# Optimization experiments

Hardware: AMD Instinct MI355X
Metric: run time of the kernel (lower is better)

The kernel has to match this reference:

```python
import jax, jax.numpy as jnp
import numpy as np

B, DEC, F = 64, 12, 32        # batch, decoder steps, decoder feature size
L, H = 2, 512                 # gru layers, hidden size
E, T = 96, 4                  # encoder seq len, target size


def gru_cell(x, h, Wi, Wh, bi, bh):
    # PyTorch GRUCell math
    gi = x @ Wi.T + bi
    gh = h @ Wh.T + bh
    i_r, i_z, i_n = jnp.split(gi, 3, axis=-1)
    h_r, h_z, h_n = jnp.split(gh, 3, axis=-1)
    r = jax.nn.sigmoid(i_r + h_r)
    z = jax.nn.sigmoid(i_z + h_z)
    n = jnp.tanh(i_n + r * h_n)
    return (1.0 - z) * n + z * h


def setup_inputs() -> dict:
    key = jax.random.key(0)
    ks = jax.random.split(key, 12)
    s = lambda k, shape: jax.random.normal(k, shape, jnp.float32) * 0.02
    return {
        "inputs": jax.random.normal(ks[0], (B, DEC, F), jnp.float32),
        "hidden": jax.random.normal(ks[1], (L, B, H), jnp.float32) * 0.1,
        "enc_outputs": jax.random.normal(ks[2], (B, E, H), jnp.float32),
        "target_indices": jnp.arange(T, dtype=jnp.int32),
        "W_attn": s(ks[3], (H, 2 * H)),
        "b_attn": jnp.zeros((H,), jnp.float32),
        "v_attn": s(ks[4], (H,)),
        "gru_Wi0": s(ks[5], (3 * H, F + H)),
        "gru_Wh0": s(ks[6], (3 * H, H)),
        "gru_bi0": jnp.zeros((3 * H,), jnp.float32),
        "gru_bh0": jnp.zeros((3 * H,), jnp.float32),
        "gru_Wi1": s(ks[7], (3 * H, H)),
        "gru_Wh1": s(ks[8], (3 * H, H)),
        "gru_bi1": jnp.zeros((3 * H,), jnp.float32),
        "gru_bh1": jnp.zeros((3 * H,), jnp.float32),
        "W_out": s(ks[9], (T, 2 * H + F)),
        "b_out": jnp.zeros((T,), jnp.float32),
    }


def reference(inputs, hidden, enc_outputs, target_indices,
              W_attn, b_attn, v_attn,
              gru_Wi0, gru_Wh0, gru_bi0, gru_bh0,
              gru_Wi1, gru_Wh1, gru_bi1, gru_bh1,
              W_out, b_out):
    Hs = hidden.shape[-1]
    Wa_h, Wa_e = W_attn[:, :Hs], W_attn[:, Hs:]
    # encoder projection of the attn linear is constant over timesteps
    enc_proj = jnp.einsum('beh,gh->beg', enc_outputs, Wa_e)  # [B,E,H]
    layers = ((gru_Wi0, gru_Wh0, gru_bi0, gru_bh0),
              (gru_Wi1, gru_Wh1, gru_bi1, gru_bh1))

    def step(carry, x_t):
        h, cur = carry                     # h: [L,B,H], cur: [B,F]
        hl = h[-1]                         # final-layer hidden [B,H]
        energy = jnp.tanh(enc_proj + (hl @ Wa_h.T + b_attn)[:, None, :])
        w = jax.nn.softmax(energy @ v_attn, axis=1)          # [B,E]
        ws = jnp.einsum('be,beh->bh', w, enc_outputs)        # [B,H]
        x = jnp.concatenate([cur, ws], axis=-1)              # [B,F+H]
        new_h = []
        for l, (Wi, Wh, bi, bh) in enumerate(layers):
            hn = gru_cell(x, h[l], Wi, Wh, bi, bh)
            new_h.append(hn)
            x = hn
        out = jnp.concatenate([x, ws, cur], axis=-1) @ W_out.T + b_out  # [B,T]
        nxt = x_t.at[:, target_indices].set(out)  # feed prediction back
        return (jnp.stack(new_h), nxt), out

    xs = jnp.swapaxes(inputs, 0, 1)  # [DEC,B,F]
    (_, _), outs = jax.lax.scan(step, (hidden, inputs[:, 0, :]), xs)
    return jnp.swapaxes(outs, 0, 1)  # [B,DEC,T]
```

## Files before the change

### kernel.cpp

```cpp
#include <hip/hip_runtime.h>
#include <hip/hip_fp16.h>

#define NB   64
#define NDEC 12
#define NF   32
#define NH   512
#define NE   96
#define NT   4
#define KI0  (NF + NH)
#define KOUT (2*NH + NF)

typedef _Float16 half8_t __attribute__((ext_vector_type(8)));
typedef float   float4_t __attribute__((ext_vector_type(4)));

__device__ __forceinline__ float fast_tanh(float x) {
    x = fminf(fmaxf(x, -15.f), 15.f);
    float e = __expf(2.f * x);
    return (e - 1.f) / (e + 1.f);
}
__device__ __forceinline__ float fast_sig(float x) {
    return 1.f / (1.f + __expf(-x));
}

__global__ __launch_bounds__(256) void k_prep(
    const float* __restrict__ Wi0, const float* __restrict__ Wh0,
    const float* __restrict__ Wi1, const float* __restrict__ Wh1,
    const float* __restrict__ Wout, const float* __restrict__ Wattn,
    const float* __restrict__ hidden, const float* __restrict__ inputs,
    __half* __restrict__ Wi0h, __half* __restrict__ Wh0h,
    __half* __restrict__ Wi1h, __half* __restrict__ Wh1h,
    __half* __restrict__ Wouth, __half* __restrict__ WahH,
    __half* __restrict__ WaeH,
    float* __restrict__ h0row, float* __restrict__ h1row,
    __half* __restrict__ h0h, __half* __restrict__ h1h,
    __half* __restrict__ xcat0)
{
    int i = blockIdx.x*256 + threadIdx.x;
    const int n0 = 1536*KI0, n1 = 1536*512, n4 = 4*KOUT, n5 = 512*512;
    if (i < n0) { Wi0h[i] = __float2half_rn(Wi0[i]); return; }  i -= n0;
    if (i < n1) { Wh0h[i] = __float2half_rn(Wh0[i]); return; }  i -= n1;
    if (i < n1) { Wi1h[i] = __float2half_rn(Wi1[i]); return; }  i -= n1;
    if (i < n1) { Wh1h[i] = __float2half_rn(Wh1[i]); return; }  i -= n1;
    if (i < n4) { Wouth[i] = __float2half_rn(Wout[i]); return; } i -= n4;
    if (i < n5) {
        int g = i >> 9, k = i & 511;
        WahH[i] = __float2half_rn(Wattn[(size_t)g*1024 + k]);
        return;
    }
    i -= n5;
    if (i < n5) {
        int g = i >> 9, k = i & 511;
        WaeH[i] = __float2half_rn(Wattn[(size_t)g*1024 + 512 + k]);
        return;
    }
    i -= n5;
    if (i < NB*NH) {
        int b = i >> 9, k = i & 511;
        float v0 = hidden[b*NH + k];
        float v1 = hidden[NB*NH + b*NH + k];
        h0row[b*NH + k] = v0;  h0h[b*NH + k] = __float2half_rn(v0);
        h1row[b*NH + k] = v1;  h1h[b*NH + k] = __float2half_rn(v1);
        return;
    }
    i -= NB*NH;
    if (i < NB*NF) {
        int b = i >> 5, k = i & 31;
        xcat0[(size_t)b*KI0 + k] = __float2half_rn(inputs[b*NDEC*NF + k]);
    }
}

__global__ __launch_bounds__(256) void k_encproj(const float* __restrict__ enc,
                                                 const __half* __restrict__ WaeH,
                                                 __half* __restrict__ encph) {
    int x = blockIdx.x;
    int by = x >> 3, bx = x & 7;
    int t = threadIdx.x, w = t >> 6, lane = t & 63;
    int mr = lane & 15, kq = lane >> 4;
    int m = by*64 + w*16 + mr;
    const float* arow = enc + (size_t)m*NH;
    float4_t acc[4] = {{0.f,0.f,0.f,0.f},{0.f,0.f,0.f,0.f},
                       {0.f,0.f,0.f,0.f},{0.f,0.f,0.f,0.f}};
    for (int kb = 0; kb < NH; kb += 32) {
        int k = kb + kq*8;
        float4 a0 = *(const float4*)(arow + k);
        float4 a1 = *(const float4*)(arow + k + 4);
        half8_t a;
        a[0] = (_Float16)a0.x; a[1] = (_Float16)a0.y;
        a[2] = (_Float16)a0.z; a[3] = (_Float16)a0.w;
        a[4] = (_Float16)a1.x; a[5] = (_Float16)a1.y;
        a[6] = (_Float16)a1.z; a[7] = (_Float16)a1.w;
        #pragma unroll
        for (int j = 0; j < 4; ++j) {
            int n = bx*64 + j*16 + mr;
            half8_t b = *(const half8_t*)(WaeH + (size_t)n*NH + k);
            acc[j] = __builtin_amdgcn_mfma_f32_16x16x32_f16(a, b, acc[j], 0, 0, 0);
        }
    }
    #pragma unroll
    for (int j = 0; j < 4; ++j) {
        int col = bx*64 + j*16 + mr;
        #pragma unroll
        for (int r = 0; r < 4; ++r) {
            int row = by*64 + w*16 + kq*4 + r;
            encph[(size_t)row*NH + col] = __float2half_rn(acc[j][r]);
        }
    }
}

__global__ __launch_bounds__(1024) void k_att(
    const __half* __restrict__ WahH, const float* __restrict__ battn,
    const __half* __restrict__ h1h,
    float* __restrict__ attcT)
{
    int blk = blockIdx.x, t = threadIdx.x;
    int w = t >> 6, lane = t & 63;
    int mr = lane & 15, kq = lane >> 4;
    int rt = (blk & 7)*4 + (blk >> 3);
    int rt16 = rt*16;
    int bq = w >> 2, wq = w & 3;
    __shared__ float parts[4][4][16][17];

    float bat = battn[rt16 + (t & 15)];
    const __half* arow = WahH + (size_t)(rt16 + mr)*NH;
    const __half* brow = h1h + (size_t)(bq*16 + mr)*NH;
    int kb0 = wq*128 + kq*8;
    half8_t a0 = *(const half8_t*)(arow + kb0);
    half8_t b0 = *(const half8_t*)(brow + kb0);
    half8_t a1 = *(const half8_t*)(arow + kb0 + 32);
    half8_t b1 = *(const half8_t*)(brow + kb0 + 32);
    half8_t a2 = *(const half8_t*)(arow + kb0 + 64);
    half8_t b2 = *(const half8_t*)(brow + kb0 + 64);
    half8_t a3 = *(const half8_t*)(arow + kb0 + 96);
    half8_t b3 = *(const half8_t*)(brow + kb0 + 96);
    float4_t acc = {0.f,0.f,0.f,0.f};
    acc = __builtin_amdgcn_mfma_f32_16x16x32_f16(a0, b0, acc, 0, 0, 0);
    acc = __builtin_amdgcn_mfma_f32_16x16x32_f16(a1, b1, acc, 0, 0, 0);
    acc = __builtin_amdgcn_mfma_f32_16x16x32_f16(a2, b2, acc, 0, 0, 0);
    acc = __builtin_amdgcn_mfma_f32_16x16x32_f16(a3, b3, acc, 0, 0, 0);
    #pragma unroll
    for (int r = 0; r < 4; ++r) parts[bq][wq][kq*4 + r][mr] = acc[r];
    __syncthreads();

    int sub = t >> 8, tt = t & 255;
    int jl = tt & 15, bl = tt >> 4;
    float v = parts[sub][0][jl][bl] + parts[sub][1][jl][bl]
            + parts[sub][2][jl][bl] + parts[sub][3][jl][bl];
    attcT[(size_t)(sub*16 + bl)*NH + rt16 + jl] = v + bat;
}

__global__ __launch_bounds__(1024) void k_soft(
    const float* __restrict__ inputs, const int* __restrict__ tgt,
    const float* __restrict__ vattn,
    const float* __restrict__ attcT,
    const __half* __restrict__ encph, const float* __restrict__ enc,
    const __half* __restrict__ Wouth, const float* __restrict__ bout,
    const __half* __restrict__ Wh0h, const __half* __restrict__ Wh1h,
    const __half* __restrict__ h0h, const __half* __restrict__ h1h,
    float* __restrict__ ghb,
    const __half* __restrict__ xcatP,
    __half* __restrict__ xcatC,
    float* __restrict__ out, int s)
{
    int blk = blockIdx.x, t = threadIdx.x;
    int lane = t & 63, widx = t >> 6;
    __shared__ float vs[NH], atts[NH];
    __shared__ float pes[NE], combA[NH], combB[NH];
    __shared__ float invD_sh;
    __shared__ float parts[4][4][16][17];

    if (blk >= 64 && blk < 256) {
        int gblk = blk - 64;
        int rt = (gblk & 7)*24 + (gblk >> 3);
        int layer = (rt >= 96) ? 1 : 0;
        int rloc = (rt - layer*96) * 16;
        int bq = widx >> 2, wq = widx & 3;
        int mr = lane & 15, kq = lane >> 4;
        const __half* Wh = layer ? Wh1h : Wh0h;
        const __half* Xh = layer ? h1h : h0h;
        const __half* arow = Wh + (size_t)(rloc + mr)*NH;
        const __half* brow = Xh + (size_t)(bq*16 + mr)*NH;
        int kb0 = wq*128 + kq*8;
        half8_t a0 = *(const half8_t*)(arow + kb0);
        half8_t b0 = *(const half8_t*)(brow + kb0);
        half8_t a1 = *(const half8_t*)(arow + kb0 + 32);
        half8_t b1 = *(const half8_t*)(brow + kb0 + 32);
        half8_t a2 = *(const half8_t*)(arow + kb0 + 64);
        half8_t b2 = *(const half8_t*)(brow + kb0 + 64);
        half8_t a3 = *(const half8_t*)(arow + kb0 + 96);
        half8_t b3 = *(const half8_t*)(brow + kb0 + 96);
        float4_t acc = {0.f,0.f,0.f,0.f};
        acc = __builtin_amdgcn_mfma_f32_16x16x32_f16(a0, b0, acc, 0, 0, 0);
        acc = __builtin_amdgcn_mfma_f32_16x16x32_f16(a1, b1, acc, 0, 0, 0);
        acc = __builtin_amdgcn_mfma_f32_16x16x32_f16(a2, b2, acc, 0, 0, 0);
        acc = __builtin_amdgcn_mfma_f32_16x16x32_f16(a3, b3, acc, 0, 0, 0);
        #pragma unroll
        for (int r = 0; r < 4; ++r) parts[bq][wq][kq*4 + r][mr] = acc[r];
        __syncthreads();
        int sub = t >> 8, tt = t & 255;
        int jl = tt >> 4, bl = tt & 15;
        float v = parts[sub][0][jl][bl] + parts[sub][1][jl][bl]
                + parts[sub][2][jl][bl] + parts[sub][3][jl][bl];
        ghb[((size_t)layer*3*NH + rloc + jl)*NB + sub*16 + bl] = v;
        return;
    }

    if (blk == 256) {
        if (s == 0 || widx >= 4) return;
        int mr = lane & 15, kq = lane >> 4;
        int b = widx*16 + mr;
        const __half* h1b = h1h + (size_t)b*NH;
        const __half* xcb = xcatP + (size_t)b*KI0;
        int ar = (mr < 4) ? mr : 3;
        const __half* arow = Wouth + (size_t)ar*KOUT;
        float4_t acc = {0.f,0.f,0.f,0.f};
        for (int kb = 0; kb < KOUT; kb += 32) {
            int k = kb + kq*8;
            half8_t a = *(const half8_t*)(arow + k);
            const __half* bp = (k < NH)   ? (h1b + k)
                             : (k < 2*NH) ? (xcb + NF + (k - NH))
                                          : (xcb + (k - 2*NH));
            half8_t bb = *(const half8_t*)bp;
            acc = __builtin_amdgcn_mfma_f32_16x16x32_f16(a, bb, acc, 0, 0, 0);
        }
        float o0 = __shfl(acc[0], mr) + bout[0];
        float o1 = __shfl(acc[1], mr) + bout[1];
        float o2 = __shfl(acc[2], mr) + bout[2];
        float o3 = __shfl(acc[3], mr) + bout[3];
        if (kq == 0) {
            *(float4*)(out + (size_t)b*(NDEC*NT) + (s-1)*NT) = make_float4(o0,o1,o2,o3);
        }
        int t0 = tgt[0], t1 = tgt[1], t2 = tgt[2], t3 = tgt[3];
        const float* ip = inputs + (size_t)b*(NDEC*NF) + (s-1)*NF;
        half8_t hv;
        #pragma unroll
        for (int i = 0; i < 8; ++i) {
            int f = kq*8 + i;
            float v = ip[f];
            v = (f == t0) ? o0 : (f == t1) ? o1 : (f == t2) ? o2 : (f == t3) ? o3 : v;
            hv[i] = (_Float16)__float2half_rn(v);
        }
        *(half8_t*)(xcatC + (size_t)b*KI0 + kq*8) = hv;
        return;
    }

    int b = blk;
    if (t < NH) { vs[t] = vattn[t]; atts[t] = attcT[(size_t)b*NH + t]; }

    float er[48];
    {
        int k = t & 511, half = t >> 9;
        const float* eb = enc + ((size_t)b*NE + half*48)*NH + k;
        #pragma unroll
        for (int e = 0; e < 48; ++e) er[e] = eb[(size_t)e*NH];
    }
    __syncthreads();

    {
        float ar[8], vr[8];
        #pragma unroll
        for (int i = 0; i < 8; ++i) { ar[i] = atts[lane*8 + i]; vr[i] = vs[lane*8 + i]; }
        for (int it = 0; it < 6; ++it) {
            int e = widx + it*16;
            const __half* ep = encph + ((size_t)(b*NE + e))*NH + lane*8;
            uint4 u = *(const uint4*)ep;
            __half2 p0 = *(__half2*)&u.x, p1 = *(__half2*)&u.y;
            __half2 p2 = *(__half2*)&u.z, p3 = *(__half2*)&u.w;
            float2 f0 = __half22float2(p0), f1 = __half22float2(p1);
            float2 f2 = __half22float2(p2), f3 = __half22float2(p3);
            float sacc;
            sacc  = fast_tanh(f0.x + ar[0]) * vr[0];
            sacc += fast_tanh(f0.y + ar[1]) * vr[1];
            sacc += fast_tanh(f1.x + ar[2]) * vr[2];
            sacc += fast_tanh(f1.y + ar[3]) * vr[3];
            sacc += fast_tanh(f2.x + ar[4]) * vr[4];
            sacc += fast_tanh(f2.y + ar[5]) * vr[5];
            sacc += fast_tanh(f3.x + ar[6]) * vr[6];
            sacc += fast_tanh(f3.y + ar[7]) * vr[7];
            #pragma unroll
            for (int off = 32; off; off >>= 1) sacc += __shfl_down(sacc, off);
            if (lane == 0) pes[e] = __expf(sacc);
        }
    }
    __syncthreads();

    if (t < 64) {
        float v = pes[t] + ((t < 32) ? pes[64 + t] : 0.f);
        #pragma unroll
        for (int off = 32; off; off >>= 1) v += __shfl_down(v, off);
        if (t == 0) invD_sh = 1.f / v;
    }
    __syncthreads();

    {
        int k = t & 511, half = t >> 9;
        float acc = 0.f;
        #pragma unroll
        for (int e = 0; e < 48; ++e) acc += pes[half*48 + e] * er[e];
        if (half == 0) combA[k] = acc; else combB[k] = acc;
    }
    __syncthreads();
    if (t < NH) {
        float v = (combA[t] + combB[t]) * invD_sh;
        xcatC[(size_t)b*KI0 + NF + t] = __float2half_rn(v);
    }
}

__global__ __launch_bounds__(768) void k_gru(
    const __half* __restrict__ Wi,
    const float* __restrict__ bi, const float* __restrict__ bh,
    const __half* __restrict__ xh, int K,
    const float* __restrict__ ghbL,
    const float* __restrict__ hold,
    float* __restrict__ hnew,
    __half* __restrict__ hnewh)
{
    int blk = blockIdx.x, t = threadIdx.x;
    int w = t >> 6, lane = t & 63;
    int mr = lane & 15, kq = lane >> 4;
    int sblk = (blk & 7)*16 + (blk >> 3);
    int jg = sblk >> 2, bq = sblk & 3;
    int j0 = jg*16, b0 = bq*16;
    __shared__ float parts[3][4][16][17];

    float ghr = 0.f, ghz = 0.f, ghn = 0.f, hp = 0.f;
    float biR = 0.f, bhR = 0.f, biZ = 0.f, bhZ = 0.f, biN = 0.f, bhN = 0.f;
    if (t < 256) {
        int jl = t >> 4, bl = t & 15;
        int j = j0 + jl, b = b0 + bl;
        ghr = ghbL[(size_t)(0*NH + j)*NB + b];
        ghz = ghbL[(size_t)(1*NH + j)*NB + b];
        ghn = ghbL[(size_t)(2*NH + j)*NB + b];
        hp  = hold[(size_t)b*NH + j];
        biR = bi[j];        bhR = bh[j];
        biZ = bi[NH + j];   bhZ = bh[NH + j];
        biN = bi[2*NH + j]; bhN = bh[2*NH + j];
    }

    int gate = w >> 2, c = w & 3;
    int nsteps = K >> 5;
    int rem = nsteps & 3;
    int base = c*(nsteps >> 2) + ((c < rem) ? c : rem);
    int cnt  = (nsteps >> 2) + ((c < rem) ? 1 : 0);
    const __half* arow = Wi + (size_t)(gate*NH + j0 + mr)*K;
    const __half* brow = xh + (size_t)(b0 + mr)*K;
    float4_t acc = {0.f,0.f,0.f,0.f};
    for (int i2 = 0; i2 < cnt; ++i2) {
        int kb = (base + i2)*32;
        half8_t a = *(const half8_t*)(arow + kb + kq*8);
        half8_t b = *(const half8_t*)(brow + kb + kq*8);
        acc = __builtin_amdgcn_mfma_f32_16x16x32_f16(a, b, acc, 0, 0, 0);
    }
    #pragma unroll
    for (int r = 0; r < 4; ++r) parts[gate][c][kq*4 + r][mr] = acc[r];
    __syncthreads();

    if (t < 256) {
        int jl = t >> 4, bl = t & 15;
        int j = j0 + jl, b = b0 + bl;
        float S0 = parts[0][0][jl][bl] + parts[0][1][jl][bl]
                 + parts[0][2][jl][bl] + parts[0][3][jl][bl];
        float S1 = parts[1][0][jl][bl] + parts[1][1][jl][bl]
                 + parts[1][2][jl][bl] + parts[1][3][jl][bl];
        float S2 = parts[2][0][jl][bl] + parts[2][1][jl][bl]
                 + parts[2][2][jl][bl] + parts[2][3][jl][bl];
        float r = fast_sig(S0 + ghr + biR + bhR);
        float z = fast_sig(S1 + ghz + biZ + bhZ);
        float n = fast_tanh(S2 + biN + r*(ghn + bhN));
        float hv = (1.f - z)*n + z*hp;
        hnew[(size_t)b*NH + j] = hv;
        hnewh[(size_t)b*NH + j] = __float2half_rn(hv);
    }
}

__global__ __launch_bounds__(256) void k_outp(
    const __half* __restrict__ Wouth, const float* __restrict__ bout,
    const __half* __restrict__ h1h, const __half* __restrict__ xcatP,
    float* __restrict__ out)
{
    int t = threadIdx.x;
    int w = t >> 6, lane = t & 63;
    int mr = lane & 15, kq = lane >> 4;
    int b = w*16 + mr;
    const __half* h1b = h1h + (size_t)b*NH;
    const __half* xcb = xcatP + (size_t)b*KI0;
    int ar = (mr < 4) ? mr : 3;
    const __half* arow = Wouth + (size_t)ar*KOUT;
    float4_t acc = {0.f,0.f,0.f,0.f};
    for (int kb = 0; kb < KOUT; kb += 32) {
        int k = kb + kq*8;
        half8_t a = *(const half8_t*)(arow + k);
        const __half* bp = (k < NH)   ? (h1b + k)
                         : (k < 2*NH) ? (xcb + NF + (k - NH))
                                      : (xcb + (k - 2*NH));
        half8_t bb = *(const half8_t*)bp;
        acc = __builtin_amdgcn_mfma_f32_16x16x32_f16(a, bb, acc, 0, 0, 0);
    }
    float o0 = __shfl(acc[0], mr) + bout[0];
    float o1 = __shfl(acc[1], mr) + bout[1];
    float o2 = __shfl(acc[2], mr) + bout[2];
    float o3 = __shfl(acc[3], mr) + bout[3];
    if (kq == 0) {
        *(float4*)(out + (size_t)b*(NDEC*NT) + (NDEC-1)*NT) = make_float4(o0,o1,o2,o3);
    }
}

extern "C" void kernel_launch(void* const* d_in, const int* in_sizes, int n_in,
                              void* d_out, int out_size, void* d_ws, size_t ws_size,
                              hipStream_t stream) {
    const float* inputs = (const float*)d_in[0];
    const float* hidden = (const float*)d_in[1];
    const float* enc    = (const float*)d_in[2];
    const int*   tgt    = (const int*)d_in[3];
    const float* Wattn  = (const float*)d_in[4];
    const float* battn  = (const float*)d_in[5];
    const float* vattn  = (const float*)d_in[6];
    const float* Wi0    = (const float*)d_in[7];
    const float* Wh0    = (const float*)d_in[8];
    const float* bi0    = (const float*)d_in[9];
    const float* bh0    = (const float*)d_in[10];
    const float* Wi1    = (const float*)d_in[11];
    const float* Wh1    = (const float*)d_in[12];
    const float* bi1    = (const float*)d_in[13];
    const float* bh1    = (const float*)d_in[14];
    const float* Wout   = (const float*)d_in[15];
    const float* bout   = (const float*)d_in[16];
    float* out = (float*)d_out;

    float* h0row  = (float*)d_ws;
    float* h1row  = h0row + NB*NH;
    float* ghb    = h1row + NB*NH;
    float* attcT  = ghb + 2*3*NH*NB;
    __half* Wi0h  = (__half*)(attcT + NB*NH);
    __half* Wh0h  = Wi0h + 1536*KI0;
    __half* Wi1h  = Wh0h + 1536*NH;
    __half* Wh1h  = Wi1h + 1536*NH;
    __half* Wouth = Wh1h + 1536*NH;
    __half* WahH  = Wouth + 4*KOUT;
    __half* WaeH  = WahH + NH*NH;
    __half* h0h   = WaeH + NH*NH;
    __half* h1h   = h0h + NB*NH;
    __half* xcat  = h1h + NB*NH;
    __half* encph = xcat + 2*NB*KI0;

    const int prep_n = 1536*KI0 + 3*1536*NH + 4*KOUT + 2*NH*NH + NB*NH + NB*NF;
    k_prep<<<(prep_n + 255)/256, 256, 0, stream>>>(
        Wi0, Wh0, Wi1, Wh1, Wout, Wattn, hidden, inputs,
        Wi0h, Wh0h, Wi1h, Wh1h, Wouth, WahH, WaeH,
        h0row, h1row, h0h, h1h, xcat);
    k_encproj<<<768, 256, 0, stream>>>(enc, WaeH, encph);

    for (int s = 0; s < NDEC; ++s) {
        int par = s & 1;
        __half* xcatC = xcat + par*NB*KI0;
        __half* xcatP = xcat + (par^1)*NB*KI0;
        k_att<<<32, 1024, 0, stream>>>(WahH, battn, h1h, attcT);
        k_soft<<<257, 1024, 0, stream>>>(
            inputs, tgt, vattn, attcT, encph, enc, Wouth, bout,
            Wh0h, Wh1h, h0h, h1h, ghb, xcatP, xcatC, out, s);
        k_gru<<<128, 768, 0, stream>>>(Wi0h, bi0, bh0,
                                       xcatC, KI0,
                                       ghb,
                                       h0row, h0row, h0h);
        k_gru<<<128, 768, 0, stream>>>(Wi1h, bi1, bh1,
                                       h0h, NH,
                                       ghb + 3*NH*NB,
                                       h1row, h1row, h1h);
    }
    k_outp<<<1, 256, 0, stream>>>(Wouth, bout, h1h, xcat + (NB*KI0), out);
}
```

Measured before the change: 485.5 us.

## Fuse attention hidden projection into softmax kernel using transposed weights

Removes the separate k_att launch per decoder step and computes each batch row's hidden-state attention projection inside the per-batch softmax block. It uses a transposed fp16 copy of the attention weight so threads read coalesced half2 pairs, with fp32 hidden values taken from shared memory. This saves one launch and one global round trip per step. In exchange, each of the 64 batch blocks now streams the full 512x512 weight matrix on its own scalar FMA path instead of using MFMA, which adds redundant L2 traffic and latency to the critical path.

Result: slower. 541.6 us (+11.6%).

```diff
diff --git a/kernel.cpp b/kernel.cpp
--- a/kernel.cpp
+++ b/kernel.cpp
@@ -29,7 +29,7 @@
     const float* __restrict__ hidden, const float* __restrict__ inputs,
     __half* __restrict__ Wi0h, __half* __restrict__ Wh0h,
     __half* __restrict__ Wi1h, __half* __restrict__ Wh1h,
-    __half* __restrict__ Wouth, __half* __restrict__ WahH,
+    __half* __restrict__ Wouth, __half* __restrict__ WahT,
     __half* __restrict__ WaeH,
     float* __restrict__ h0row, float* __restrict__ h1row,
     __half* __restrict__ h0h, __half* __restrict__ h1h,
@@ -43,8 +43,8 @@
     if (i < n1) { Wh1h[i] = __float2half_rn(Wh1[i]); return; }  i -= n1;
     if (i < n4) { Wouth[i] = __float2half_rn(Wout[i]); return; } i -= n4;
     if (i < n5) {
-        int g = i >> 9, k = i & 511;
-        WahH[i] = __float2half_rn(Wattn[(size_t)g*1024 + k]);
+        int k = i >> 9, g = i & 511;
+        WahT[i] = __float2half_rn(Wattn[(size_t)g*1024 + k]);
         return;
     }
     i -= n5;
@@ -107,51 +107,11 @@
     }
 }
 
-__global__ __launch_bounds__(1024) void k_att(
-    const __half* __restrict__ WahH, const float* __restrict__ battn,
-    const __half* __restrict__ h1h,
-    float* __restrict__ attcT)
-{
-    int blk = blockIdx.x, t = threadIdx.x;
-    int w = t >> 6, lane = t & 63;
-    int mr = lane & 15, kq = lane >> 4;
-    int rt = (blk & 7)*4 + (blk >> 3);
-    int rt16 = rt*16;
-    int bq = w >> 2, wq = w & 3;
-    __shared__ float parts[4][4][16][17];
-
-    float bat = battn[rt16 + (t & 15)];
-    const __half* arow = WahH + (size_t)(rt16 + mr)*NH;
-    const __half* brow = h1h + (size_t)(bq*16 + mr)*NH;
-    int kb0 = wq*128 + kq*8;
-    half8_t a0 = *(const half8_t*)(arow + kb0);
-    half8_t b0 = *(const half8_t*)(brow + kb0);
-    half8_t a1 = *(const half8_t*)(arow + kb0 + 32);
-    half8_t b1 = *(const half8_t*)(brow + kb0 + 32);
-    half8_t a2 = *(const half8_t*)(arow + kb0 + 64);
-    half8_t b2 = *(const half8_t*)(brow + kb0 + 64);
-    half8_t a3 = *(const half8_t*)(arow + kb0 + 96);
-    half8_t b3 = *(const half8_t*)(brow + kb0 + 96);
-    float4_t acc = {0.f,0.f,0.f,0.f};
-    acc = __builtin_amdgcn_mfma_f32_16x16x32_f16(a0, b0, acc, 0, 0, 0);
-    acc = __builtin_amdgcn_mfma_f32_16x16x32_f16(a1, b1, acc, 0, 0, 0);
-    acc = __builtin_amdgcn_mfma_f32_16x16x32_f16(a2, b2, acc, 0, 0, 0);
-    acc = __builtin_amdgcn_mfma_f32_16x16x32_f16(a3, b3, acc, 0, 0, 0);
-    #pragma unroll
-    for (int r = 0; r < 4; ++r) parts[bq][wq][kq*4 + r][mr] = acc[r];
-    __syncthreads();
-
-    int sub = t >> 8, tt = t & 255;
-    int jl = tt & 15, bl = tt >> 4;
-    float v = parts[sub][0][jl][bl] + parts[sub][1][jl][bl]
-            + parts[sub][2][jl][bl] + parts[sub][3][jl][bl];
-    attcT[(size_t)(sub*16 + bl)*NH + rt16 + jl] = v + bat;
-}
-
 __global__ __launch_bounds__(1024) void k_soft(
     const float* __restrict__ inputs, const int* __restrict__ tgt,
-    const float* __restrict__ vattn,
-    const float* __restrict__ attcT,
+    const __half* __restrict__ WahT,
+    const float* __restrict__ battn, const float* __restrict__ vattn,
+    const float* __restrict__ h1row,
     const __half* __restrict__ encph, const float* __restrict__ enc,
     const __half* __restrict__ Wouth, const float* __restrict__ bout,
     const __half* __restrict__ Wh0h, const __half* __restrict__ Wh1h,
@@ -163,7 +123,8 @@
 {
     int blk = blockIdx.x, t = threadIdx.x;
     int lane = t & 63, widx = t >> 6;
-    __shared__ float vs[NH], atts[NH];
+    __shared__ float h1s[NH], vs[NH], atts[NH];
+    __shared__ float2 attp2[4][256];
     __shared__ float pes[NE], combA[NH], combB[NH];
     __shared__ float invD_sh;
     __shared__ float parts[4][4][16][17];
@@ -244,7 +205,7 @@
     }
 
     int b = blk;
-    if (t < NH) { vs[t] = vattn[t]; atts[t] = attcT[(size_t)b*NH + t]; }
+    if (t < NH) { h1s[t] = h1row[(size_t)b*NH + t]; vs[t] = vattn[t]; }
 
     float er[48];
     {
@@ -252,6 +213,28 @@
         const float* eb = enc + ((size_t)b*NE + half*48)*NH + k;
         #pragma unroll
         for (int e = 0; e < 48; ++e) er[e] = eb[(size_t)e*NH];
+    }
+    __syncthreads();
+
+    {
+        int g2 = t & 255, kqa = t >> 8;
+        float a0 = 0.f, a1 = 0.f;
+        #pragma unroll 4
+        for (int k = kqa*128; k < kqa*128 + 128; ++k) {
+            float2 f = __half22float2(*(const __half2*)(WahT + (size_t)k*NH + g2*2));
+            float h = h1s[k];
+            a0 += f.x*h; a1 += f.y*h;
+        }
+        attp2[kqa][g2] = make_float2(a0, a1);
+    }
+    __syncthreads();
+    if (t < NH) {
+        int g = t;
+        float2 p0 = attp2[0][g>>1], p1 = attp2[1][g>>1];
+        float2 p2 = attp2[2][g>>1], p3 = attp2[3][g>>1];
+        float v = (g & 1) ? (p0.y + p1.y + p2.y + p3.y)
+                          : (p0.x + p1.x + p2.x + p3.x);
+        atts[g] = v + battn[g];
     }
     __syncthreads();
 
@@ -429,14 +412,13 @@
     float* h0row  = (float*)d_ws;
     float* h1row  = h0row + NB*NH;
     float* ghb    = h1row + NB*NH;
-    float* attcT  = ghb + 2*3*NH*NB;
-    __half* Wi0h  = (__half*)(attcT + NB*NH);
+    __half* Wi0h  = (__half*)(ghb + 2*3*NH*NB);
     __half* Wh0h  = Wi0h + 1536*KI0;
     __half* Wi1h  = Wh0h + 1536*NH;
     __half* Wh1h  = Wi1h + 1536*NH;
     __half* Wouth = Wh1h + 1536*NH;
-    __half* WahH  = Wouth + 4*KOUT;
-    __half* WaeH  = WahH + NH*NH;
+    __half* WahT  = Wouth + 4*KOUT;
+    __half* WaeH  = WahT + NH*NH;
     __half* h0h   = WaeH + NH*NH;
     __half* h1h   = h0h + NB*NH;
     __half* xcat  = h1h + NB*NH;
@@ -445,7 +427,7 @@
     const int prep_n = 1536*KI0 + 3*1536*NH + 4*KOUT + 2*NH*NH + NB*NH + NB*NF;
     k_prep<<<(prep_n + 255)/256, 256, 0, stream>>>(
         Wi0, Wh0, Wi1, Wh1, Wout, Wattn, hidden, inputs,
-        Wi0h, Wh0h, Wi1h, Wh1h, Wouth, WahH, WaeH,
+        Wi0h, Wh0h, Wi1h, Wh1h, Wouth, WahT, WaeH,
         h0row, h1row, h0h, h1h, xcat);
     k_encproj<<<768, 256, 0, stream>>>(enc, WaeH, encph);
 
@@ -453,10 +435,9 @@
         int par = s & 1;
         __half* xcatC = xcat + par*NB*KI0;
         __half* xcatP = xcat + (par^1)*NB*KI0;
-        k_att<<<32, 1024, 0, stream>>>(WahH, battn, h1h, attcT);
         k_soft<<<257, 1024, 0, stream>>>(
-            inputs, tgt, vattn, attcT, encph, enc, Wouth, bout,
-            Wh0h, Wh1h, h0h, h1h, ghb, xcatP, xcatC, out, s);
+            inputs, tgt, WahT, battn, vattn, h1row, encph, enc,
+            Wouth, bout, Wh0h, Wh1h, h0h, h1h, ghb, xcatP, xcatC, out, s);
         k_gru<<<128, 768, 0, stream>>>(Wi0h, bi0, bh0,
                                        xcatC, KI0,
                                        ghb,
```
